# Optimization experiments

Hardware: AMD Instinct MI355X
Metric: run time of the kernel (lower is better)

Reference implementation:

```python
import jax, jax.numpy as jnp
import numpy as np

H, HKV, D, HID = 32, 8, 128, 4096
L, CTX, S = 64, 64, 8192
T = CTX + L
HALF = D // 2
EPS = 1e-6
WP = 4096


def setup_inputs() -> dict:
    key = jax.random.key(0)
    ks = jax.random.split(key, 16)
    f = jnp.float32
    w = 0.02
    return {
        "x": jax.random.normal(ks[0], (1, L, HID), f),
        "x_ctx": jax.random.normal(ks[1], (1, CTX, HID), f),
        "cos_q": jax.random.uniform(ks[2], (1, 1, L, HALF), f, -1.0, 1.0),
        "sin_q": jax.random.uniform(ks[3], (1, 1, L, HALF), f, -1.0, 1.0),
        "cos_k": jax.random.uniform(ks[4], (1, 1, T, HALF), f, -1.0, 1.0),
        "sin_k": jax.random.uniform(ks[5], (1, 1, T, HALF), f, -1.0, 1.0),
        "cache_K_in": jax.random.normal(ks[6], (1, HKV, S, D), f),
        "cache_V_in": jax.random.normal(ks[7], (1, HKV, S, D), f),
        "causal_mask": jnp.ones((1, 1, L, WP + T), dtype=bool),
        "Wq": jax.random.normal(ks[8], (HID, H * D), f) * w,
        "Wk": jax.random.normal(ks[9], (HID, HKV * D), f) * w,
        "Wv": jax.random.normal(ks[10], (HID, HKV * D), f) * w,
        "Wo": jax.random.normal(ks[11], (H * D, HID), f) * w,
        "q_norm_w": jnp.ones((D,), f),
        "k_norm_w": jnp.ones((D,), f),
        "write_pos": WP,
        "rotate": 0,
    }


def _rmsnorm(x, w):
    # normalize over head_dim (last axis)
    var = jnp.mean(x * x, axis=-1, keepdims=True)
    return x * jax.lax.rsqrt(var + EPS) * w


def _rope(x, cos, sin):
    # x: (B, H, T, D); cos/sin: (1, 1, T, HALF) -- rotate-half convention
    x1, x2 = x[..., :HALF], x[..., HALF:]
    return jnp.concatenate([x1 * cos - x2 * sin, x2 * cos + x1 * sin], axis=-1)


def reference(x, x_ctx, cos_q, sin_q, cos_k, sin_k, cache_K_in, cache_V_in,
              causal_mask, Wq, Wk, Wv, Wo, q_norm_w, k_norm_w, write_pos, rotate):
    c = jnp.concatenate([x_ctx, x], axis=1)                  # (1, T, HID)
    q = (x @ Wq).reshape(1, L, H, D)
    k = (c @ Wk).reshape(1, T, HKV, D)
    v = (c @ Wv).reshape(1, T, HKV, D)
    q = _rmsnorm(q, q_norm_w).transpose(0, 2, 1, 3)          # (1, H, L, D)
    k = _rmsnorm(k, k_norm_w).transpose(0, 2, 1, 3)          # (1, HKV, T, D)
    v = v.transpose(0, 2, 1, 3)                               # (1, HKV, T, D)
    q = _rope(q, cos_q, sin_q)
    k = _rope(k, cos_k, sin_k)

    if rotate:  # static Python branch (rotate is a compile-time constant)
        attend_K = jnp.concatenate([cache_K_in[:, :, T:S], k], axis=2)
        attend_V = jnp.concatenate([cache_V_in[:, :, T:S], v], axis=2)
    elif write_pos == 0:
        attend_K, attend_V = k, v
    else:
        attend_K = jnp.concatenate([cache_K_in[:, :, :write_pos], k], axis=2)
        attend_V = jnp.concatenate([cache_V_in[:, :, :write_pos], v], axis=2)

    rep = H // HKV
    scale = jnp.float32(D) ** -0.5
    qg = q.reshape(1, HKV, rep, L, D)
    # grouped attention: broadcast KV heads inline instead of materializing expand
    scores = jnp.einsum('bgrld,bgad->bgrla', qg, attend_K) * scale
    scores = jnp.where(causal_mask[:, :, None], scores, -jnp.inf)  # (1,1,1,L,A) bcast
    probs = jax.nn.softmax(scores, axis=-1)
    o = jnp.einsum('bgrla,bgad->bgrld', probs, attend_V)     # (1, HKV, rep, L, D)
    o = o.reshape(1, H, L, D).transpose(0, 2, 1, 3).reshape(1, L, H * D)
    return (o @ Wo, k, v)
```

## Files before the change

### kernel.cpp

```cpp
#include <hip/hip_runtime.h>

typedef unsigned short u16;
typedef __bf16 bf16x8 __attribute__((ext_vector_type(8)));
typedef float f32x4 __attribute__((ext_vector_type(4)));
typedef u16 u16x8 __attribute__((ext_vector_type(8)));

#define NSPLIT 11
#define ANBLK 6
#define KSPLIT 8
#define OSPLIT 8
#define SCALE_Q 0.08838834764831843f

__device__ __forceinline__ u16 f2bf(float f) {
    unsigned u = __builtin_bit_cast(unsigned, f);
    u += 0x7fff + ((u >> 16) & 1);
    return (u16)(u >> 16);
}
__device__ __forceinline__ float bf2f(u16 h) {
    unsigned u = ((unsigned)h) << 16;
    return __builtin_bit_cast(float, u);
}
__device__ __forceinline__ f32x4 mfma16(bf16x8 a, bf16x8 b, f32x4 c) {
    return __builtin_amdgcn_mfma_f32_16x16x32_bf16(a, b, c, 0, 0, 0);
}

__global__ __launch_bounds__(256)
void k_prep(const float* __restrict__ x, const float* __restrict__ xctx,
            u16* __restrict__ fragA)
{
    int tid = blockIdx.x * 256 + threadIdx.x;
    int row = tid >> 9;
    int k0 = (tid & 511) << 3;
    const float* src = (row < 64) ? (xctx + (size_t)row * 4096)
                                  : (x + (size_t)(row - 64) * 4096);
    f32x4 v0 = *(const f32x4*)&src[k0];
    f32x4 v1 = *(const f32x4*)&src[k0 + 4];
    u16x8 o;
    o[0] = f2bf(v0[0]); o[1] = f2bf(v0[1]); o[2] = f2bf(v0[2]); o[3] = f2bf(v0[3]);
    o[4] = f2bf(v1[0]); o[5] = f2bf(v1[1]); o[6] = f2bf(v1[2]); o[7] = f2bf(v1[3]);
    int ks32 = k0 >> 5;
    int lg = (k0 >> 3) & 3;
    int rt = row >> 4;
    int l = lg * 16 + (row & 15);
    *(u16x8*)&fragA[(((size_t)ks32 * 8 + rt) * 64 + l) * 8] = o;
}

template<int KS>
__global__ __launch_bounds__(256)
void k_qkv(const u16* __restrict__ fragA,
           const float* __restrict__ Wq, const float* __restrict__ Wk,
           const float* __restrict__ Wv, float* __restrict__ part)
{
    constexpr int KCk = 4096 / KS;
    constexpr int NKTk = KCk / 64;
    const int col0 = blockIdx.x * 32;
    const int ksp = blockIdx.y;
    const int ks0 = ksp * KCk;
    const float* W; int ldw, cbase, mat;
    if (col0 < 4096)      { W = Wq; ldw = 4096; cbase = col0;        mat = 0; }
    else if (col0 < 5120) { W = Wk; ldw = 1024; cbase = col0 - 4096; mat = 1; }
    else                  { W = Wv; ldw = 1024; cbase = col0 - 5120; mat = 2; }
    const bool full = (mat != 0);
    const int rowbase = full ? 0 : 64;

    __shared__ __align__(16) u16 Bs[2][32 * 64];

    const int t = threadIdx.x;
    const int w = t >> 6, l = t & 63;
    const int lm = l & 15, lg = l >> 4;
    const int bk = (t >> 3) << 1;
    const int bn4 = (t & 7) << 2;

    f32x4 pb[2];
    f32x4 acc[2][2] = {};
    const int rt0 = full ? (w * 2) : (4 + w);

    #define QKV_BLOAD(kt_)                                                     \
    {                                                                          \
        const int kg = ks0 + (kt_) * 64;                                       \
        pb[0] = *(const f32x4*)&W[(size_t)(kg + bk) * ldw + cbase + bn4];      \
        pb[1] = *(const f32x4*)&W[(size_t)(kg + bk + 1) * ldw + cbase + bn4];  \
    }
    #define QKV_BSTORE(buf_)                                                   \
    {                                                                          \
        _Pragma("unroll")                                                      \
        for (int j = 0; j < 4; j++) {                                          \
            int n = bn4 + j;                                                   \
            int idx = n * 64 + (bk ^ (((n >> 1) & 7) << 3));                   \
            ushort2 v2; v2.x = f2bf(pb[0][j]); v2.y = f2bf(pb[1][j]);          \
            *(ushort2*)&Bs[buf_][idx] = v2;                                    \
        }                                                                      \
    }

    QKV_BLOAD(0);
    QKV_BSTORE(0);
    __syncthreads();
    if (NKTk > 1) QKV_BLOAD(1);
    #pragma unroll 1
    for (int kt = 0; kt < NKTk; kt++) {
        const int cur = kt & 1;
        const int ks32b = (ks0 >> 5) + kt * 2;
        #pragma unroll
        for (int ks = 0; ks < 2; ks++) {
            const int koff = ks * 32 + lg * 8;
            bf16x8 bfr[2];
            #pragma unroll
            for (int nt = 0; nt < 2; nt++) {
                int n = nt * 16 + lm;
                bfr[nt] = *(const bf16x8*)
                    &Bs[cur][n * 64 + (koff ^ (((n >> 1) & 7) << 3))];
            }
            bf16x8 a0 = *(const bf16x8*)
                &fragA[(((size_t)(ks32b + ks) * 8 + rt0) * 64 + l) * 8];
            acc[0][0] = mfma16(a0, bfr[0], acc[0][0]);
            acc[0][1] = mfma16(a0, bfr[1], acc[0][1]);
            if (full) {
                bf16x8 a1 = *(const bf16x8*)
                    &fragA[(((size_t)(ks32b + ks) * 8 + rt0 + 1) * 64 + l) * 8];
                acc[1][0] = mfma16(a1, bfr[0], acc[1][0]);
                acc[1][1] = mfma16(a1, bfr[1], acc[1][1]);
            }
        }
        if (kt + 1 < NKTk) {
            QKV_BSTORE(cur ^ 1);
            if (kt + 2 < NKTk) QKV_BLOAD(kt + 2);
            __syncthreads();
        }
    }

    const int wrows = full ? 32 : 16;
    const int mts = full ? 2 : 1;
    #pragma unroll
    for (int mt = 0; mt < 2; mt++) {
        if (mt >= mts) break;
        #pragma unroll
        for (int nt = 0; nt < 2; nt++)
            #pragma unroll
            for (int r = 0; r < 4; r++) {
                int grow = rowbase + w * wrows + mt * 16 + lg * 4 + r;
                part[((size_t)ksp * 128 + grow) * 6144 + col0 + nt * 16 + lm] =
                    acc[mt][nt][r];
            }
    }
    #undef QKV_BLOAD
    #undef QKV_BSTORE
}

template<int KS>
__global__ __launch_bounds__(256)
void k_normrope(const float* __restrict__ part,
                const float* __restrict__ cosq, const float* __restrict__ sinq,
                const float* __restrict__ cosk, const float* __restrict__ sink,
                const float* __restrict__ qnw, const float* __restrict__ knw,
                u16* __restrict__ qb, u16* __restrict__ kb,
                float* __restrict__ outk, float* __restrict__ outv,
                u16* __restrict__ vbw)
{
    int wid = blockIdx.x * 4 + (threadIdx.x >> 6);
    int lane = threadIdx.x & 63;
    if (wid < 2048) {
        int h = wid >> 6, lq = wid & 63;
        size_t ro = (size_t)(64 + lq) * 6144 + h * 128;
        float x1 = 0.f, x2 = 0.f;
        #pragma unroll
        for (int s = 0; s < KS; s++) {
            x1 += part[(size_t)s * 786432 + ro + lane];
            x2 += part[(size_t)s * 786432 + ro + lane + 64];
        }
        float ss = x1 * x1 + x2 * x2;
        #pragma unroll
        for (int off = 32; off; off >>= 1) ss += __shfl_xor(ss, off);
        float rms = rsqrtf(ss * (1.0f / 128.0f) + 1e-6f);
        float a = x1 * rms * qnw[lane];
        float b = x2 * rms * qnw[lane + 64];
        float c = cosq[lq * 64 + lane], s = sinq[lq * 64 + lane];
        u16* qo = qb + ((size_t)h * 64 + lq) * 128;
        qo[lane]      = f2bf((a * c - b * s) * SCALE_Q);
        qo[lane + 64] = f2bf((b * c + a * s) * SCALE_Q);
    } else if (wid < 3072) {
        int rr = wid - 2048;
        int kh = rr >> 7, tt = rr & 127;
        size_t ro = (size_t)tt * 6144 + 4096 + kh * 128;
        float x1 = 0.f, x2 = 0.f;
        #pragma unroll
        for (int s = 0; s < KS; s++) {
            x1 += part[(size_t)s * 786432 + ro + lane];
            x2 += part[(size_t)s * 786432 + ro + lane + 64];
        }
        float ss = x1 * x1 + x2 * x2;
        #pragma unroll
        for (int off = 32; off; off >>= 1) ss += __shfl_xor(ss, off);
        float rms = rsqrtf(ss * (1.0f / 128.0f) + 1e-6f);
        float a = x1 * rms * knw[lane];
        float b = x2 * rms * knw[lane + 64];
        float c = cosk[tt * 64 + lane], s = sink[tt * 64 + lane];
        float o1 = a * c - b * s, o2 = b * c + a * s;
        size_t oi = ((size_t)kh * 128 + tt) * 128;
        outk[oi + lane] = o1; outk[oi + lane + 64] = o2;
        kb[oi + lane] = f2bf(o1); kb[oi + lane + 64] = f2bf(o2);
    } else {
        int rr = wid - 3072;
        int kh = rr >> 7, tt = rr & 127;
        size_t ro = (size_t)tt * 6144 + 5120 + kh * 128;
        float v1 = 0.f, v2 = 0.f;
        #pragma unroll
        for (int s = 0; s < KS; s++) {
            v1 += part[(size_t)s * 786432 + ro + lane];
            v2 += part[(size_t)s * 786432 + ro + lane + 64];
        }
        size_t oi = ((size_t)kh * 128 + tt) * 128;
        outv[oi + lane] = v1; outv[oi + lane + 64] = v2;
        vbw[oi + lane] = f2bf(v1); vbw[oi + lane + 64] = f2bf(v2);
    }
}

__global__ __launch_bounds__(256)
void k_prepkv(const float* __restrict__ cacheK, const float* __restrict__ cacheV,
              const u16* __restrict__ kb, const u16* __restrict__ vb,
              u16* __restrict__ kc, u16* __restrict__ vt)
{
    const int bx = blockIdx.x;
    const int t = threadIdx.x;
    if (bx < 528) {
        __shared__ __align__(16) u16 Ls[64][132];
        int kh = bx / 66, tile = bx % 66;
        int key0 = tile * 64;
        #pragma unroll
        for (int it = 0; it < 8; it++) {
            int fidx = it * 256 + t;
            int row = fidx >> 5;
            int d4 = (fidx & 31) << 2;
            int key = key0 + row;
            ushort4 sv;
            if (key < 4096) {
                float4 v = *(const float4*)&cacheV[((size_t)kh * 8192 + key) * 128 + d4];
                sv.x = f2bf(v.x); sv.y = f2bf(v.y); sv.z = f2bf(v.z); sv.w = f2bf(v.w);
            } else {
                sv = *(const ushort4*)&vb[((size_t)kh * 128 + (key - 4096)) * 128 + d4];
            }
            *(ushort4*)&Ls[row][d4] = sv;
        }
        __syncthreads();
        #pragma unroll
        for (int it = 0; it < 4; it++) {
            int fidx = it * 256 + t;
            int d = fidx >> 3;
            int kc8 = (fidx & 7) << 3;
            u16x8 o;
            #pragma unroll
            for (int j = 0; j < 8; j++) o[j] = Ls[kc8 + j][d];
            *(u16x8*)&vt[((size_t)kh * 128 + d) * 4224 + key0 + kc8] = o;
        }
    } else {
        size_t cidx = (size_t)(bx - 528) * 256 + t;
        int kh = (int)(cidx / 67584);
        int rem = (int)(cidx % 67584);
        int tt = rem >> 4;
        int d8 = (rem & 15) << 3;
        u16x8 o;
        if (tt < 4096) {
            const float* src = &cacheK[((size_t)kh * 8192 + tt) * 128 + d8];
            f32x4 a = *(const f32x4*)src;
            f32x4 b = *(const f32x4*)(src + 4);
            o[0] = f2bf(a[0]); o[1] = f2bf(a[1]); o[2] = f2bf(a[2]); o[3] = f2bf(a[3]);
            o[4] = f2bf(b[0]); o[5] = f2bf(b[1]); o[6] = f2bf(b[2]); o[7] = f2bf(b[3]);
        } else {
            o = *(const u16x8*)&kb[((size_t)kh * 128 + (tt - 4096)) * 128 + d8];
        }
        *(u16x8*)&kc[((size_t)kh * 4224 + tt) * 128 + d8] = o;
    }
}

__global__ __launch_bounds__(256)
void k_attn(const u16* __restrict__ qb, const u16* __restrict__ kcache,
            const u16* __restrict__ vcacheT,
            u16* __restrict__ opart, float* __restrict__ lpart)
{
    const int split = blockIdx.x;
    const int kh = blockIdx.y;
    const int z = blockIdx.z;
    const int t = threadIdx.x;
    const int w = t >> 6, l = t & 63;
    const int lm = l & 15, lg = l >> 4;
    const int rep = z * 2 + (w >> 1);
    const int mh = w & 1;

    __shared__ __align__(16) u16 Ks[64][136];
    __shared__ __align__(16) u16 Vs[128][72];
    __shared__ __align__(16) u16 Ps[4][32][40];

    const u16* qh = qb + ((size_t)(kh * 4 + rep) * 64) * 128;
    bf16x8 aq[2][4];
    #pragma unroll
    for (int mt = 0; mt < 2; mt++)
        #pragma unroll
        for (int ks = 0; ks < 4; ks++)
            aq[mt][ks] = *(const bf16x8*)
                &qh[(size_t)(mh * 32 + mt * 16 + lm) * 128 + ks * 32 + lg * 8];

    const u16* kcb = kcache + (size_t)kh * 4224 * 128;
    const u16* vtb = vcacheT + (size_t)kh * 128 * 4224;

    const int krow = t >> 4;
    const int kdc = (t & 15) << 3;
    const int vd = t >> 3;
    const int vkc = t & 7;

    u16x8 pk[4], pv[4];
    f32x4 accO[2][8] = {};
    float lacc[2][4] = {};

    #define AT_LOAD(key0_)                                                     \
    {                                                                          \
        _Pragma("unroll")                                                      \
        for (int it = 0; it < 4; it++)                                         \
            pk[it] = *(const u16x8*)&kcb[(size_t)((key0_) + it * 16 + krow) * 128 + kdc]; \
        _Pragma("unroll")                                                      \
        for (int it = 0; it < 4; it++)                                         \
            pv[it] = *(const u16x8*)&vtb[(size_t)(it * 32 + vd) * 4224 + (key0_) + vkc * 8]; \
    }
    #define AT_STORE()                                                         \
    {                                                                          \
        _Pragma("unroll")                                                      \
        for (int it = 0; it < 4; it++)                                         \
            *(u16x8*)&Ks[it * 16 + krow][kdc] = pk[it];                        \
        _Pragma("unroll")                                                      \
        for (int it = 0; it < 4; it++) {                                       \
            int d = it * 32 + vd;                                              \
            *(u16x8*)&Vs[d][(vkc ^ ((d >> 2) & 7)) << 3] = pv[it];             \
        }                                                                      \
    }

    AT_LOAD(split * (64 * ANBLK));
    #pragma unroll 1
    for (int kbi = 0; kbi < ANBLK; kbi++) {
        __syncthreads();
        AT_STORE();
        __syncthreads();
        if (kbi + 1 < ANBLK) AT_LOAD(split * (64 * ANBLK) + (kbi + 1) * 64);

        f32x4 sa[2][4] = {};
        #pragma unroll
        for (int ks = 0; ks < 4; ks++) {
            bf16x8 bk[4];
            #pragma unroll
            for (int nt = 0; nt < 4; nt++)
                bk[nt] = *(const bf16x8*)&Ks[nt * 16 + lm][ks * 32 + lg * 8];
            #pragma unroll
            for (int mt = 0; mt < 2; mt++)
                #pragma unroll
                for (int nt = 0; nt < 4; nt++)
                    sa[mt][nt] = mfma16(aq[mt][ks], bk[nt], sa[mt][nt]);
        }

        #pragma unroll
        for (int half = 0; half < 2; half++) {
            #pragma unroll
            for (int mt = 0; mt < 2; mt++)
                #pragma unroll
                for (int nt2 = 0; nt2 < 2; nt2++)
                    #pragma unroll
                    for (int r = 0; r < 4; r++) {
                        float e = __expf(sa[mt][half * 2 + nt2][r]);
                        lacc[mt][r] += e;
                        Ps[w][mt * 16 + lg * 4 + r][nt2 * 16 + lm] = f2bf(e);
                    }
            bf16x8 pa[2];
            #pragma unroll
            for (int mt = 0; mt < 2; mt++)
                pa[mt] = *(const bf16x8*)&Ps[w][mt * 16 + lm][lg * 8];
            #pragma unroll
            for (int dt = 0; dt < 8; dt++) {
                int d = dt * 16 + lm;
                int vswz = ((d >> 2) & 7) << 3;
                bf16x8 vb8 = *(const bf16x8*)&Vs[d][(half * 32 + lg * 8) ^ vswz];
                #pragma unroll
                for (int mt = 0; mt < 2; mt++)
                    accO[mt][dt] = mfma16(pa[mt], vb8, accO[mt][dt]);
            }
        }
    }
    #undef AT_LOAD
    #undef AT_STORE

    #pragma unroll
    for (int mt = 0; mt < 2; mt++)
        #pragma unroll
        for (int r = 0; r < 4; r++) {
            float v = lacc[mt][r];
            v += __shfl_xor(v, 1);
            v += __shfl_xor(v, 2);
            v += __shfl_xor(v, 4);
            v += __shfl_xor(v, 8);
            lacc[mt][r] = v;
        }

    const size_t base = (((size_t)kh * NSPLIT + split) * 4 + rep) * 64 + mh * 32;
    if (lm == 0) {
        #pragma unroll
        for (int mt = 0; mt < 2; mt++)
            #pragma unroll
            for (int r = 0; r < 4; r++)
                lpart[base + mt * 16 + lg * 4 + r] = lacc[mt][r];
    }
    #pragma unroll
    for (int mt = 0; mt < 2; mt++)
        #pragma unroll
        for (int dt = 0; dt < 8; dt++)
            #pragma unroll
            for (int r = 0; r < 4; r++)
                opart[(base + mt * 16 + lg * 4 + r) * 128 + dt * 16 + lm] =
                    f2bf(accO[mt][dt][r]);
}

template<int NSP>
__global__ __launch_bounds__(256)
void k_combine(const u16* __restrict__ opart, const float* __restrict__ lpart,
               u16* __restrict__ obf)
{
    int idx = blockIdx.x * 256 + threadIdx.x;
    int lq = idx >> 9;
    int c8 = (idx & 511) << 3;
    int h = c8 >> 7, d = c8 & 127;
    int kh = h >> 2, rep = h & 3;
    float os[8] = {};
    float ls = 0.f;
    #pragma unroll
    for (int s = 0; s < NSP; s++) {
        size_t b = (((size_t)kh * NSP + s) * 4 + rep) * 64 + lq;
        u16x8 v = *(const u16x8*)&opart[b * 128 + d];
        #pragma unroll
        for (int j = 0; j < 8; j++) os[j] += bf2f(v[j]);
        ls += lpart[b];
    }
    float inv = 1.0f / ls;
    u16x8 o;
    #pragma unroll
    for (int j = 0; j < 8; j++) o[j] = f2bf(os[j] * inv);
    *(u16x8*)&obf[(size_t)lq * 4096 + c8] = o;
}

__global__ __launch_bounds__(256)
void k_oproj(const u16* __restrict__ obf, const float* __restrict__ Wo,
             float* __restrict__ parto)
{
    constexpr int NKT = 4096 / OSPLIT / 64;
    const int col0 = blockIdx.x * 32;
    const int osp = blockIdx.y;
    const int ks0 = osp * (4096 / OSPLIT);

    __shared__ __align__(16) u16 As[2][64][72];
    __shared__ __align__(16) u16 Bs[2][32 * 64];

    const int t = threadIdx.x;
    const int w = t >> 6, l = t & 63;
    const int lm = l & 15, lg = l >> 4;

    const int arow = t >> 3;
    const int ac8 = (t & 7) << 3;
    const int bk = (t >> 3) << 1;
    const int bn4 = (t & 7) << 2;

    u16x8 pa[2]; f32x4 pb[2];
    f32x4 acc[2] = {};

    #define OP_LOAD(kt_)                                                       \
    {                                                                          \
        const int kg = ks0 + (kt_) * 64;                                       \
        pa[0] = *(const u16x8*)&obf[(size_t)arow * 4096 + kg + ac8];           \
        pa[1] = *(const u16x8*)&obf[(size_t)(arow + 32) * 4096 + kg + ac8];    \
        pb[0] = *(const f32x4*)&Wo[(size_t)(kg + bk) * 4096 + col0 + bn4];     \
        pb[1] = *(const f32x4*)&Wo[(size_t)(kg + bk + 1) * 4096 + col0 + bn4]; \
    }
    #define OP_STORE(buf_)                                                     \
    {                                                                          \
        *(u16x8*)&As[buf_][arow][ac8] = pa[0];                                 \
        *(u16x8*)&As[buf_][arow + 32][ac8] = pa[1];                            \
        _Pragma("unroll")                                                      \
        for (int j = 0; j < 4; j++) {                                          \
            int n = bn4 + j;                                                   \
            int idx = n * 64 + (bk ^ (((n >> 1) & 7) << 3));                   \
            ushort2 v2; v2.x = f2bf(pb[0][j]); v2.y = f2bf(pb[1][j]);          \
            *(ushort2*)&Bs[buf_][idx] = v2;                                    \
        }                                                                      \
    }

    OP_LOAD(0);
    OP_STORE(0);
    __syncthreads();
    OP_LOAD(1);
    #pragma unroll 1
    for (int kt = 0; kt < NKT; kt++) {
        const int cur = kt & 1;
        #pragma unroll
        for (int ks = 0; ks < 2; ks++) {
            const int koff = ks * 32 + lg * 8;
            bf16x8 a0 = *(const bf16x8*)&As[cur][w * 16 + lm][koff];
            #pragma unroll
            for (int nt = 0; nt < 2; nt++) {
                int n = nt * 16 + lm;
                bf16x8 b = *(const bf16x8*)
                    &Bs[cur][n * 64 + (koff ^ (((n >> 1) & 7) << 3))];
                acc[nt] = mfma16(a0, b, acc[nt]);
            }
        }
        if (kt + 1 < NKT) {
            OP_STORE(cur ^ 1);
            if (kt + 2 < NKT) OP_LOAD(kt + 2);
            __syncthreads();
        }
    }
    #pragma unroll
    for (int nt = 0; nt < 2; nt++)
        #pragma unroll
        for (int r = 0; r < 4; r++)
            parto[((size_t)osp * 64 + w * 16 + lg * 4 + r) * 4096 +
                  col0 + nt * 16 + lm] = acc[nt][r];
    #undef OP_LOAD
    #undef OP_STORE
}

__global__ __launch_bounds__(256)
void k_osum(const float* __restrict__ parto, float* __restrict__ out0)
{
    int idx = blockIdx.x * 256 + threadIdx.x;
    float s = 0.f;
    #pragma unroll
    for (int o = 0; o < OSPLIT; o++)
        s += parto[(size_t)o * 262144 + idx];
    out0[idx] = s;
}

extern "C" void kernel_launch(void* const* d_in, const int* in_sizes, int n_in,
                              void* d_out, int out_size, void* d_ws, size_t ws_size,
                              hipStream_t stream)
{
    (void)in_sizes; (void)n_in; (void)out_size; (void)ws_size;
    const float* x      = (const float*)d_in[0];
    const float* xctx   = (const float*)d_in[1];
    const float* cosq   = (const float*)d_in[2];
    const float* sinq   = (const float*)d_in[3];
    const float* cosk   = (const float*)d_in[4];
    const float* sink   = (const float*)d_in[5];
    const float* cacheK = (const float*)d_in[6];
    const float* cacheV = (const float*)d_in[7];
    const float* Wq     = (const float*)d_in[9];
    const float* Wk     = (const float*)d_in[10];
    const float* Wv     = (const float*)d_in[11];
    const float* Wo     = (const float*)d_in[12];
    const float* qnw    = (const float*)d_in[13];
    const float* knw    = (const float*)d_in[14];

    float* out0 = (float*)d_out;
    float* out1 = out0 + 262144;
    float* out2 = out1 + 131072;

    char* ws = (char*)d_ws;
    float* part  = (float*)(ws + 0);
    u16*   kc    = (u16*)(ws + 0);
    u16*   vt    = (u16*)(ws + 8650752);
    u16*   opart = (u16*)(ws + 17301504);
    float* lpart = (float*)(ws + 23068672);
    float* parto = (float*)(ws + 0);
    u16*   fragA = (u16*)(ws + 25165824);
    u16*   qb    = (u16*)(ws + 25165824);
    u16*   kb    = (u16*)(ws + 25165824 + 524288);
    u16*   vb    = (u16*)(ws + 25165824 + 786432);
    u16*   obf   = (u16*)(ws + 25165824 + 1048576);

    k_prep<<<256, 256, 0, stream>>>(x, xctx, fragA);
    k_qkv<KSPLIT><<<dim3(192, KSPLIT), 256, 0, stream>>>(fragA, Wq, Wk, Wv, part);
    k_normrope<KSPLIT><<<1024, 256, 0, stream>>>(part, cosq, sinq, cosk, sink,
                                                 qnw, knw, qb, kb, out1, out2, vb);
    k_prepkv<<<2640, 256, 0, stream>>>(cacheK, cacheV, kb, vb, kc, vt);
    k_attn<<<dim3(NSPLIT, 8, 2), 256, 0, stream>>>(qb, kc, vt, opart, lpart);
    k_combine<NSPLIT><<<128, 256, 0, stream>>>(opart, lpart, obf);
    k_oproj<<<dim3(128, OSPLIT), 256, 0, stream>>>(obf, Wo, parto);
    k_osum<<<1024, 256, 0, stream>>>(parto, out0);
}
```

Baseline: 80.57 us.

## Deepen global prefetch to four stages in QKV and output GEMMs, halve QKV k-split

The QKV and output-projection GEMMs now keep four k-tiles of global weight loads in flight in registers instead of one, and the loops are fully unrolled. In the QKV kernel the A fragments are also prefetched one tile ahead in registers. KSPLIT drops from 8 to 4, so each QKV block does twice the k-work over fewer blocks and writes fewer partials for the norm/rope stage to reduce. The aim is to hide global load latency better, at the cost of more registers and possibly lower occupancy and less parallelism.

Result: faster. 77.44 us, median of 2 (-3.9%).

```diff
diff --git a/kernel.cpp b/kernel.cpp
--- a/kernel.cpp
+++ b/kernel.cpp
@@ -7,7 +7,7 @@
 
 #define NSPLIT 11
 #define ANBLK 6
-#define KSPLIT 8
+#define KSPLIT 4
 #define OSPLIT 8
 #define SCALE_Q 0.08838834764831843f
 
@@ -52,7 +52,7 @@
            const float* __restrict__ Wv, float* __restrict__ part)
 {
     constexpr int KCk = 4096 / KS;
-    constexpr int NKTk = KCk / 64;
+    constexpr int NKT = KCk / 64;
     const int col0 = blockIdx.x * 32;
     const int ksp = blockIdx.y;
     const int ks0 = ksp * KCk;
@@ -71,35 +71,52 @@
     const int bk = (t >> 3) << 1;
     const int bn4 = (t & 7) << 2;
 
-    f32x4 pb[2];
+    f32x4 pb[4][2];
+    bf16x8 af[2][4];
     f32x4 acc[2][2] = {};
     const int rt0 = full ? (w * 2) : (4 + w);
 
-    #define QKV_BLOAD(kt_)                                                     \
+    #define QKV_BLOAD(slot_, kt_)                                              \
     {                                                                          \
         const int kg = ks0 + (kt_) * 64;                                       \
-        pb[0] = *(const f32x4*)&W[(size_t)(kg + bk) * ldw + cbase + bn4];      \
-        pb[1] = *(const f32x4*)&W[(size_t)(kg + bk + 1) * ldw + cbase + bn4];  \
-    }
-    #define QKV_BSTORE(buf_)                                                   \
+        pb[slot_][0] = *(const f32x4*)&W[(size_t)(kg + bk) * ldw + cbase + bn4]; \
+        pb[slot_][1] = *(const f32x4*)&W[(size_t)(kg + bk + 1) * ldw + cbase + bn4]; \
+    }
+    #define QKV_BSTORE(buf_, slot_)                                            \
     {                                                                          \
         _Pragma("unroll")                                                      \
         for (int j = 0; j < 4; j++) {                                          \
             int n = bn4 + j;                                                   \
             int idx = n * 64 + (bk ^ (((n >> 1) & 7) << 3));                   \
-            ushort2 v2; v2.x = f2bf(pb[0][j]); v2.y = f2bf(pb[1][j]);          \
+            ushort2 v2; v2.x = f2bf(pb[slot_][0][j]); v2.y = f2bf(pb[slot_][1][j]); \
             *(ushort2*)&Bs[buf_][idx] = v2;                                    \
         }                                                                      \
     }
-
-    QKV_BLOAD(0);
-    QKV_BSTORE(0);
+    #define QKV_ALOAD(p_, kt_)                                                 \
+    {                                                                          \
+        const int kb32 = (ks0 >> 5) + (kt_) * 2;                               \
+        af[p_][0] = *(const bf16x8*)&fragA[(((size_t)kb32 * 8 + rt0) * 64 + l) * 8]; \
+        af[p_][1] = *(const bf16x8*)&fragA[(((size_t)(kb32 + 1) * 8 + rt0) * 64 + l) * 8]; \
+        if (full) {                                                            \
+            af[p_][2] = *(const bf16x8*)&fragA[(((size_t)kb32 * 8 + rt0 + 1) * 64 + l) * 8]; \
+            af[p_][3] = *(const bf16x8*)&fragA[(((size_t)(kb32 + 1) * 8 + rt0 + 1) * 64 + l) * 8]; \
+        }                                                                      \
+    }
+
+    QKV_BLOAD(0, 0);
+    QKV_BLOAD(1, 1);
+    QKV_BLOAD(2, 2);
+    QKV_BLOAD(3, 3);
+    QKV_ALOAD(0, 0);
+    QKV_BSTORE(0, 0);
     __syncthreads();
-    if (NKTk > 1) QKV_BLOAD(1);
-    #pragma unroll 1
-    for (int kt = 0; kt < NKTk; kt++) {
+
+    #pragma unroll
+    for (int kt = 0; kt < NKT; kt++) {
         const int cur = kt & 1;
-        const int ks32b = (ks0 >> 5) + kt * 2;
+        if (kt + 4 < NKT) QKV_BLOAD(kt & 3, kt + 4);
+        if (kt + 1 < NKT) QKV_ALOAD((kt + 1) & 1, kt + 1);
+        if (kt + 1 < NKT) QKV_BSTORE(cur ^ 1, (kt + 1) & 3);
         #pragma unroll
         for (int ks = 0; ks < 2; ks++) {
             const int koff = ks * 32 + lg * 8;
@@ -110,22 +127,14 @@
                 bfr[nt] = *(const bf16x8*)
                     &Bs[cur][n * 64 + (koff ^ (((n >> 1) & 7) << 3))];
             }
-            bf16x8 a0 = *(const bf16x8*)
-                &fragA[(((size_t)(ks32b + ks) * 8 + rt0) * 64 + l) * 8];
-            acc[0][0] = mfma16(a0, bfr[0], acc[0][0]);
-            acc[0][1] = mfma16(a0, bfr[1], acc[0][1]);
+            acc[0][0] = mfma16(af[cur][ks], bfr[0], acc[0][0]);
+            acc[0][1] = mfma16(af[cur][ks], bfr[1], acc[0][1]);
             if (full) {
-                bf16x8 a1 = *(const bf16x8*)
-                    &fragA[(((size_t)(ks32b + ks) * 8 + rt0 + 1) * 64 + l) * 8];
-                acc[1][0] = mfma16(a1, bfr[0], acc[1][0]);
-                acc[1][1] = mfma16(a1, bfr[1], acc[1][1]);
+                acc[1][0] = mfma16(af[cur][2 + ks], bfr[0], acc[1][0]);
+                acc[1][1] = mfma16(af[cur][2 + ks], bfr[1], acc[1][1]);
             }
         }
-        if (kt + 1 < NKTk) {
-            QKV_BSTORE(cur ^ 1);
-            if (kt + 2 < NKTk) QKV_BLOAD(kt + 2);
-            __syncthreads();
-        }
+        if (kt + 1 < NKT) __syncthreads();
     }
 
     const int wrows = full ? 32 : 16;
@@ -144,6 +153,7 @@
     }
     #undef QKV_BLOAD
     #undef QKV_BSTORE
+    #undef QKV_ALOAD
 }
 
 template<int KS>
@@ -461,37 +471,43 @@
     const int bk = (t >> 3) << 1;
     const int bn4 = (t & 7) << 2;
 
-    u16x8 pa[2]; f32x4 pb[2];
+    u16x8 pa[4][2];
+    f32x4 pb[4][2];
     f32x4 acc[2] = {};
 
-    #define OP_LOAD(kt_)                                                       \
+    #define OP_LOAD(slot_, kt_)                                                \
     {                                                                          \
         const int kg = ks0 + (kt_) * 64;                                       \
-        pa[0] = *(const u16x8*)&obf[(size_t)arow * 4096 + kg + ac8];           \
-        pa[1] = *(const u16x8*)&obf[(size_t)(arow + 32) * 4096 + kg + ac8];    \
-        pb[0] = *(const f32x4*)&Wo[(size_t)(kg + bk) * 4096 + col0 + bn4];     \
-        pb[1] = *(const f32x4*)&Wo[(size_t)(kg + bk + 1) * 4096 + col0 + bn4]; \
-    }
-    #define OP_STORE(buf_)                                                     \
-    {                                                                          \
-        *(u16x8*)&As[buf_][arow][ac8] = pa[0];                                 \
-        *(u16x8*)&As[buf_][arow + 32][ac8] = pa[1];                            \
+        pa[slot_][0] = *(const u16x8*)&obf[(size_t)arow * 4096 + kg + ac8];    \
+        pa[slot_][1] = *(const u16x8*)&obf[(size_t)(arow + 32) * 4096 + kg + ac8]; \
+        pb[slot_][0] = *(const f32x4*)&Wo[(size_t)(kg + bk) * 4096 + col0 + bn4]; \
+        pb[slot_][1] = *(const f32x4*)&Wo[(size_t)(kg + bk + 1) * 4096 + col0 + bn4]; \
+    }
+    #define OP_STORE(buf_, slot_)                                              \
+    {                                                                          \
+        *(u16x8*)&As[buf_][arow][ac8] = pa[slot_][0];                          \
+        *(u16x8*)&As[buf_][arow + 32][ac8] = pa[slot_][1];                     \
         _Pragma("unroll")                                                      \
         for (int j = 0; j < 4; j++) {                                          \
             int n = bn4 + j;                                                   \
             int idx = n * 64 + (bk ^ (((n >> 1) & 7) << 3));                   \
-            ushort2 v2; v2.x = f2bf(pb[0][j]); v2.y = f2bf(pb[1][j]);          \
+            ushort2 v2; v2.x = f2bf(pb[slot_][0][j]); v2.y = f2bf(pb[slot_][1][j]); \
             *(ushort2*)&Bs[buf_][idx] = v2;                                    \
         }                                                                      \
     }
 
-    OP_LOAD(0);
-    OP_STORE(0);
+    OP_LOAD(0, 0);
+    OP_LOAD(1, 1);
+    OP_LOAD(2, 2);
+    OP_LOAD(3, 3);
+    OP_STORE(0, 0);
     __syncthreads();
-    OP_LOAD(1);
-    #pragma unroll 1
+
+    #pragma unroll
     for (int kt = 0; kt < NKT; kt++) {
         const int cur = kt & 1;
+        if (kt + 4 < NKT) OP_LOAD(kt & 3, kt + 4);
+        if (kt + 1 < NKT) OP_STORE(cur ^ 1, (kt + 1) & 3);
         #pragma unroll
         for (int ks = 0; ks < 2; ks++) {
             const int koff = ks * 32 + lg * 8;
@@ -504,11 +520,7 @@
                 acc[nt] = mfma16(a0, b, acc[nt]);
             }
         }
-        if (kt + 1 < NKT) {
-            OP_STORE(cur ^ 1);
-            if (kt + 2 < NKT) OP_LOAD(kt + 2);
-            __syncthreads();
-        }
+        if (kt + 1 < NKT) __syncthreads();
     }
     #pragma unroll
     for (int nt = 0; nt < 2; nt++)
```
